# Kernel optimization log

Hardware: AMD Instinct MI355X
Metric: run time of the kernel (lower is better)

The kernel has to match this reference:

```python
import jax, jax.numpy as jnp
import numpy as np

N_NODES = 50000
N_EDGES = 800000
IN_FEATS = 128
H_FEATS = 32
HEADS = 4
OUT_FEATS = 32
OUT_HEADS = 1
NEG_SLOPE = 0.2


def setup_inputs() -> dict:
    key = jax.random.key(0)
    ks = jax.random.split(key, 20)
    s = 0.05
    return {
        "features": jax.random.normal(ks[0], (N_NODES, IN_FEATS), jnp.float32),
        "src": jax.random.randint(ks[1], (N_EDGES,), 0, N_NODES, jnp.int32),
        "dst": jax.random.randint(ks[2], (N_EDGES,), 0, N_NODES, jnp.int32),
        "Ws0": jax.random.normal(ks[3], (IN_FEATS, HEADS * H_FEATS), jnp.float32) * s,
        "bs0": jnp.zeros((HEADS * H_FEATS,), jnp.float32),
        "Wd0": jax.random.normal(ks[4], (IN_FEATS, HEADS * H_FEATS), jnp.float32) * s,
        "bd0": jnp.zeros((HEADS * H_FEATS,), jnp.float32),
        "a0": jax.random.normal(ks[5], (HEADS, H_FEATS), jnp.float32) * s,
        "Ws1": jax.random.normal(ks[6], (HEADS * H_FEATS, HEADS * H_FEATS), jnp.float32) * s,
        "bs1": jnp.zeros((HEADS * H_FEATS,), jnp.float32),
        "Wd1": jax.random.normal(ks[7], (HEADS * H_FEATS, HEADS * H_FEATS), jnp.float32) * s,
        "bd1": jnp.zeros((HEADS * H_FEATS,), jnp.float32),
        "a1": jax.random.normal(ks[8], (HEADS, H_FEATS), jnp.float32) * s,
        "Ws2": jax.random.normal(ks[9], (HEADS * H_FEATS, OUT_HEADS * OUT_FEATS), jnp.float32) * s,
        "bs2": jnp.zeros((OUT_HEADS * OUT_FEATS,), jnp.float32),
        "Wd2": jax.random.normal(ks[10], (HEADS * H_FEATS, OUT_HEADS * OUT_FEATS), jnp.float32) * s,
        "bd2": jnp.zeros((OUT_HEADS * OUT_FEATS,), jnp.float32),
        "a2": jax.random.normal(ks[11], (OUT_HEADS, OUT_FEATS), jnp.float32) * s,
    }


def gatv2_conv(x, src, dst, Ws, bs, Wd, bd, attn, n_nodes):
    """DGL GATv2Conv (share_weights=False, residual=False, no dropout)."""
    heads, f = attn.shape
    feat_src = (x @ Ws + bs).reshape(-1, heads, f)  # [N, H, F]
    feat_dst = (x @ Wd + bd).reshape(-1, heads, f)  # [N, H, F]
    # per-edge GATv2 score: LeakyReLU(Wsrc h_u + Wdst h_v) . a
    e = jax.nn.leaky_relu(feat_src[src] + feat_dst[dst], NEG_SLOPE)  # [E, H, F]
    logits = jnp.einsum("ehf,hf->eh", e, attn)  # [E, H]
    # edge softmax over incoming edges of each dst node
    m = jax.ops.segment_max(logits, dst, num_segments=n_nodes)  # [N, H]
    ex = jnp.exp(logits - m[dst])
    denom = jax.ops.segment_sum(ex, dst, num_segments=n_nodes)  # [N, H]
    alpha = ex / denom[dst]  # [E, H]
    # scatter-aggregate messages
    msg = feat_src[src] * alpha[..., None]  # [E, H, F]
    return jax.ops.segment_sum(msg, dst, num_segments=n_nodes)  # [N, H, F]


def reference(features, src, dst,
              Ws0, bs0, Wd0, bd0, a0,
              Ws1, bs1, Wd1, bd1, a1,
              Ws2, bs2, Wd2, bd2, a2):
    n = features.shape[0]
    h = gatv2_conv(features, src, dst, Ws0, bs0, Wd0, bd0, a0, n)
    h = jax.nn.relu(h.reshape(n, -1))
    h = gatv2_conv(h, src, dst, Ws1, bs1, Wd1, bd1, a1, n)
    h = jax.nn.relu(h.reshape(n, -1))
    h = gatv2_conv(h, src, dst, Ws2, bs2, Wd2, bd2, a2, n)
    return h.mean(axis=1)  # [N, OUT_FEATS]
```

## Files before the change

### kernel.cpp

```cpp
#include <hip/hip_runtime.h>

typedef __attribute__((ext_vector_type(8))) short bf16x8;
typedef __attribute__((ext_vector_type(4))) float f32x4;

#define LOG2E 1.4426950408889634f

#define BINSH 8
#define NBIN 196
#define CHUNK 4096
#define K4CAP 6144

__device__ __forceinline__ unsigned bf_rn(float f) {
    unsigned u = __float_as_uint(f);
    u += 0x7fffu + ((u >> 16) & 1u);
    return u >> 16;
}
__device__ __forceinline__ float bf_lo(unsigned u) { return __uint_as_float(u << 16); }
__device__ __forceinline__ float bf_hi(unsigned u) { return __uint_as_float(u & 0xffff0000u); }

template <int CTRL>
__device__ __forceinline__ float dpp_radd(float x) {
    int t = __builtin_amdgcn_update_dpp(0, __float_as_int(x), CTRL, 0xF, 0xF, true);
    return x + __int_as_float(t);
}
__device__ __forceinline__ float sum8(float p) {
    p = dpp_radd<0x141>(p);
    p = dpp_radd<0x1B>(p);
    p = dpp_radd<0xB1>(p);
    return p;
}
__device__ __forceinline__ float dpp_swap1(float x) {
    return __int_as_float(__builtin_amdgcn_update_dpp(0, __float_as_int(x), 0xB1, 0xF, 0xF, true));
}

__device__ __forceinline__ float fast_exp2(float x) {
#if __has_builtin(__builtin_amdgcn_exp2f)
    return __builtin_amdgcn_exp2f(x);
#else
    return __expf(x * 0.6931471805599453f);
#endif
}


__global__ __launch_bounds__(256) void bin_count(const int* __restrict__ dst,
                                                 int* __restrict__ binCnt, int e) {
    __shared__ int hist[NBIN];
    for (int t = threadIdx.x; t < NBIN; t += 256) hist[t] = 0;
    __syncthreads();
    int base = blockIdx.x * CHUNK;
    int cnt = min(CHUNK, e - base);
    for (int j = threadIdx.x; j < cnt; j += 256)
        atomicAdd(&hist[dst[base + j] >> BINSH], 1);
    __syncthreads();
    for (int t = threadIdx.x; t < NBIN; t += 256)
        if (hist[t]) atomicAdd(&binCnt[t], hist[t]);
}

__global__ void bin_scan(const int* __restrict__ binCnt, int* __restrict__ binBase,
                         int* __restrict__ binCur, int* __restrict__ rowp, int n, int e) {
    int t = threadIdx.x;
    int v = (t < NBIN) ? binCnt[t] : 0;
    int lane = t & 63, w = t >> 6;
    int incl = v;
    for (int off = 1; off < 64; off <<= 1) {
        int tt = __shfl_up(incl, off);
        if (lane >= off) incl += tt;
    }
    __shared__ int wsum[4];
    if (lane == 63) wsum[w] = incl;
    __syncthreads();
    int wpre = 0;
    for (int i = 0; i < w; ++i) wpre += wsum[i];
    int excl = wpre + incl - v;
    if (t < NBIN) { binBase[t] = excl; binCur[t] = excl; }
    if (t == 0) { binBase[NBIN] = e; rowp[n] = e; }
}

__global__ __launch_bounds__(256) void bin_scatter(
    const int* __restrict__ src, const int* __restrict__ dst,
    int* __restrict__ binCur, unsigned* __restrict__ ebin, int e) {
    __shared__ int hist[NBIN];
    __shared__ int seg[NBIN];
    __shared__ int gbase[NBIN];
    __shared__ unsigned pack[CHUNK];
    for (int t = threadIdx.x; t < NBIN; t += 256) hist[t] = 0;
    __syncthreads();
    int base = blockIdx.x * CHUNK;
    int cnt = min(CHUNK, e - base);

    int myb[CHUNK / 256], myr[CHUNK / 256];
    unsigned myw[CHUNK / 256];
    int nmine = 0;
    for (int j = threadIdx.x; j < cnt; j += 256) {
        int d = dst[base + j], s = src[base + j];
        int b = d >> BINSH, dl = d & ((1 << BINSH) - 1);
        int r = atomicAdd(&hist[b], 1);
        myb[nmine] = b; myr[nmine] = r;
        myw[nmine] = ((unsigned)b << 24) | ((unsigned)dl << 16) | (unsigned)s;
        ++nmine;
    }
    __syncthreads();
    if (threadIdx.x == 0) {
        int acc = 0;
        for (int b2 = 0; b2 < NBIN; ++b2) { seg[b2] = acc; acc += hist[b2]; }
    }
    __syncthreads();
    for (int k = 0; k < nmine; ++k)
        pack[seg[myb[k]] + myr[k]] = myw[k];
    __syncthreads();
    if (threadIdx.x < NBIN && hist[threadIdx.x])
        gbase[threadIdx.x] = atomicAdd(&binCur[threadIdx.x], hist[threadIdx.x]);
    __syncthreads();
    for (int j = threadIdx.x; j < cnt; j += 256) {
        unsigned wv = pack[j];
        int b = wv >> 24;
        ebin[gbase[b] + (j - seg[b])] = wv;
    }
}

__global__ __launch_bounds__(256) void csr_build(
    const unsigned* __restrict__ ebin, const int* __restrict__ binBase,
    int* __restrict__ rowp, int* __restrict__ csrc, int n) {
    __shared__ int hist[256];
    __shared__ int seg[256];
    __shared__ unsigned stage[K4CAP];
    int b = blockIdx.x;
    int e0 = binBase[b], e1 = binBase[b + 1];
    int n0 = b << BINSH;
    int nn = min(256, n - n0);
    for (int t = threadIdx.x; t < 256; t += 256) hist[t] = 0;
    __syncthreads();
    for (int i = e0 + threadIdx.x; i < e1; i += 256) {
        unsigned wv = ebin[i];
        atomicAdd(&hist[(wv >> 16) & 255], 1);
        int off = i - e0;
        if (off < K4CAP) stage[off] = wv;
    }
    __syncthreads();
    if (threadIdx.x < 64) {
        int l = threadIdx.x;
        int s = 0, loc[4];
#pragma unroll
        for (int k = 0; k < 4; ++k) { loc[k] = s; s += hist[l * 4 + k]; }
        int incl = s;
        for (int off = 1; off < 64; off <<= 1) {
            int tt = __shfl_up(incl, off);
            if (l >= off) incl += tt;
        }
        int excl = incl - s;
#pragma unroll
        for (int k = 0; k < 4; ++k) seg[l * 4 + k] = excl + loc[k];
    }
    __syncthreads();
    for (int t = threadIdx.x; t < nn; t += 256) rowp[n0 + t] = e0 + seg[t];
    for (int t = threadIdx.x; t < 256; t += 256) hist[t] = seg[t];
    __syncthreads();
    for (int i = e0 + threadIdx.x; i < e1; i += 256) {
        int off = i - e0;
        unsigned wv = (off < K4CAP) ? stage[off] : ebin[i];
        int dl = (wv >> 16) & 255;
        int pos = e0 + atomicAdd(&hist[dl], 1);
        csrc[pos] = (int)(wv & 0xFFFFu);
    }
}


__global__ void convert_feat(const float* __restrict__ x, unsigned short* __restrict__ o, int n4) {
    int i = blockIdx.x * blockDim.x + threadIdx.x;
    if (i < n4) {
        float4 v = *(const float4*)(x + (size_t)i * 4);
        ushort4 r;
        r.x = (unsigned short)bf_rn(v.x); r.y = (unsigned short)bf_rn(v.y);
        r.z = (unsigned short)bf_rn(v.z); r.w = (unsigned short)bf_rn(v.w);
        *(ushort4*)(o + (size_t)i * 4) = r;
    }
}

__global__ void transpose_all(
    const float* __restrict__ Ws0, const float* __restrict__ Wd0,
    const float* __restrict__ Ws1, const float* __restrict__ Wd1,
    const float* __restrict__ Ws2, const float* __restrict__ Wd2,
    unsigned short* __restrict__ wt0, unsigned short* __restrict__ wt1,
    unsigned short* __restrict__ wt2) {
    int gid = blockIdx.x * blockDim.x + threadIdx.x;
    if (gid < 65536) {
        int l = gid >> 15, loc = gid & 32767;
        int c = loc >> 7, k = loc & 127;
        const float* W = (c < 128) ? (l ? Ws1 : Ws0) : (l ? Wd1 : Wd0);
        int cc = c & 127;
        float v = W[(size_t)k * 128 + cc];
        (l ? wt1 : wt0)[loc] = (unsigned short)bf_rn(v);
    } else if (gid < 65536 + 8192) {
        int loc = gid - 65536;
        int c = loc >> 7, k = loc & 127;
        const float* W = (c < 32) ? Ws2 : Wd2;
        int cc = (c < 32) ? c : c - 32;
        float v = W[(size_t)k * 32 + cc];
        wt2[loc] = (unsigned short)bf_rn(v);
    }
}


template <int COLS2>
__global__ __launch_bounds__(256) void gemm_dual2(
    const unsigned short* __restrict__ xb, const unsigned short* __restrict__ wt,
    const float* __restrict__ bs, const float* __restrict__ bd,
    unsigned short* __restrict__ fs, unsigned short* __restrict__ fd,
    int n, int nch) {
    constexpr int C  = COLS2 / 2;
    constexpr int NC = COLS2 / 64;

    const int lane = threadIdx.x & 63;
    const int m = lane & 15, quad = lane >> 4;
    const int gwid = blockIdx.x * 4 + (threadIdx.x >> 6);
    const int nwaves = gridDim.x * 4;
    const int cs = gwid % NC;
    const int cstride = nwaves / NC;

    float biasv[4];
#pragma unroll
    for (int ct = 0; ct < 4; ++ct) {
        int col = cs * 64 + ct * 16 + m;
        biasv[ct] = (col < C) ? bs[col] : bd[col - C];
    }

    for (int chunk = gwid / NC; chunk < nch; chunk += cstride) {
        const size_t r0 = (size_t)chunk * 64;

        f32x4 acc[4][4];
#pragma unroll
        for (int rt = 0; rt < 4; ++rt)
#pragma unroll
            for (int ct = 0; ct < 4; ++ct) acc[rt][ct] = (f32x4){0.f, 0.f, 0.f, 0.f};

#pragma unroll
        for (int ks = 0; ks < 4; ++ks) {
            const int ko = ks * 32 + quad * 8;
            bf16x8 a[4], b[4];
#pragma unroll
            for (int rt = 0; rt < 4; ++rt)
                a[rt] = *(const bf16x8*)(xb + (r0 + rt * 16 + m) * 128 + ko);
#pragma unroll
            for (int ct = 0; ct < 4; ++ct)
                b[ct] = *(const bf16x8*)(wt + (size_t)(cs * 64 + ct * 16 + m) * 128 + ko);
#pragma unroll
            for (int rt = 0; rt < 4; ++rt)
#pragma unroll
                for (int ct = 0; ct < 4; ++ct)
                    acc[rt][ct] = __builtin_amdgcn_mfma_f32_16x16x32_bf16(a[rt], b[ct], acc[rt][ct], 0, 0, 0);
        }

        const int odd = m & 1;
#pragma unroll
        for (int ct = 0; ct < 4; ++ct) {
            int colE = cs * 64 + ct * 16 + (m & ~1);
            unsigned short* ptr = (colE < C) ? fs : fd;
            int cc = (colE < C) ? colE : colE - C;
#pragma unroll
            for (int rt = 0; rt < 4; ++rt) {
                float v0 = acc[rt][ct][0] + biasv[ct];
                float v1 = acc[rt][ct][1] + biasv[ct];
                float v2 = acc[rt][ct][2] + biasv[ct];
                float v3 = acc[rt][ct][3] + biasv[ct];
                float s0 = dpp_swap1(v0), s1 = dpp_swap1(v1);
                float s2 = dpp_swap1(v2), s3 = dpp_swap1(v3);
                float aLo = odd ? s2 : v0, aHi = odd ? v2 : s0;
                float bLo = odd ? s3 : v1, bHi = odd ? v3 : s1;
                int rowA = (int)r0 + rt * 16 + quad * 4 + (odd ? 2 : 0);
                unsigned pa = (bf_rn(aHi) << 16) | bf_rn(aLo);
                unsigned pb = (bf_rn(bHi) << 16) | bf_rn(bLo);
                if (rowA < n)     *(unsigned*)(ptr + (size_t)rowA * C + cc)       = pa;
                if (rowA + 1 < n) *(unsigned*)(ptr + ((size_t)rowA + 1) * C + cc) = pb;
            }
        }
    }
}


#define EDGE_BODY(u, mval)                                          \
    do {                                                            \
        float x0 = bf_lo((u).x), x1 = bf_hi((u).x);                 \
        float x2 = bf_lo((u).y), x3 = bf_hi((u).y);                 \
        float t0 = x0 + fd0, t1 = x1 + fd1;                         \
        float t2 = x2 + fd2, t3 = x3 + fd3;                         \
        float p = a060 * t0;                                        \
        p = fmaf(a040, fabsf(t0), p);                               \
        p = fmaf(a061, t1, p); p = fmaf(a041, fabsf(t1), p);        \
        p = fmaf(a062, t2, p); p = fmaf(a042, fabsf(t2), p);        \
        p = fmaf(a063, t3, p); p = fmaf(a043, fabsf(t3), p);        \
        p = sum8(p);                                                \
        float ex = fast_exp2(p) * (mval);                           \
        denom += ex;                                                \
        acc0 = fmaf(ex, x0, acc0); acc1 = fmaf(ex, x1, acc1);       \
        acc2 = fmaf(ex, x2, acc2); acc3 = fmaf(ex, x3, acc3);       \
    } while (0)

__global__ __launch_bounds__(256) void conv128(
    const unsigned short* __restrict__ fs, const unsigned short* __restrict__ fd,
    const float* __restrict__ attn, const int* __restrict__ rowp,
    const int* __restrict__ csrc, unsigned short* __restrict__ out, int n) {
    const int nwaves = gridDim.x * 4;
    const int wid0 = blockIdx.x * 4 + (threadIdx.x >> 6);
    const int lane = threadIdx.x & 63;
    const int half = lane >> 5;
    const int q = lane & 31;

    float4 av = *(const float4*)(attn + q * 4);
    const float a060 = av.x * 0.6f * LOG2E, a040 = av.x * 0.4f * LOG2E;
    const float a061 = av.y * 0.6f * LOG2E, a041 = av.y * 0.4f * LOG2E;
    const float a062 = av.z * 0.6f * LOG2E, a042 = av.z * 0.4f * LOG2E;
    const float a063 = av.w * 0.6f * LOG2E, a043 = av.w * 0.4f * LOG2E;

    for (int wid = wid0; wid < n; wid += nwaves) {
        uint2 ud = *(const uint2*)(fd + (size_t)wid * 128 + q * 4);
        float fd0 = bf_lo(ud.x), fd1 = bf_hi(ud.x);
        float fd2 = bf_lo(ud.y), fd3 = bf_hi(ud.y);
        int rs = rowp[wid], re = rowp[wid + 1];
        float acc0 = 0.f, acc1 = 0.f, acc2 = 0.f, acc3 = 0.f, denom = 0.f;

        int i = rs;
        for (; i + 3 < re; i += 4) {
            int sA = csrc[i + half];
            int sB = csrc[i + 2 + half];
            uint2 uA = *(const uint2*)(fs + ((size_t)sA << 7) + q * 4);
            uint2 uB = *(const uint2*)(fs + ((size_t)sB << 7) + q * 4);
            EDGE_BODY(uA, 1.0f);
            EDGE_BODY(uB, 1.0f);
        }
        for (; i + 1 < re; i += 2) {
            int s = csrc[i + half];
            uint2 u = *(const uint2*)(fs + ((size_t)s << 7) + q * 4);
            EDGE_BODY(u, 1.0f);
        }
        if (i < re) {
            int s = csrc[i];
            uint2 u = *(const uint2*)(fs + ((size_t)s << 7) + q * 4);
            float mval = half ? 0.f : 1.f;
            EDGE_BODY(u, mval);
        }
        acc0 += __shfl_xor(acc0, 32); acc1 += __shfl_xor(acc1, 32);
        acc2 += __shfl_xor(acc2, 32); acc3 += __shfl_xor(acc3, 32);
        denom += __shfl_xor(denom, 32);
        float inv = (re > rs) ? 1.f / denom : 0.f;
        float r0 = fmaxf(acc0 * inv, 0.f), r1 = fmaxf(acc1 * inv, 0.f);
        float r2 = fmaxf(acc2 * inv, 0.f), r3 = fmaxf(acc3 * inv, 0.f);
        if (half == 0) {
            uint2 o;
            o.x = (bf_rn(r1) << 16) | bf_rn(r0);
            o.y = (bf_rn(r3) << 16) | bf_rn(r2);
            ((uint2*)(out + (size_t)wid * 128))[q] = o;
        }
    }
}

__global__ __launch_bounds__(256) void conv32(
    const unsigned short* __restrict__ fs, const unsigned short* __restrict__ fd,
    const float* __restrict__ attn, const int* __restrict__ rowp,
    const int* __restrict__ csrc, float* __restrict__ out, int n) {
    const int nwaves = gridDim.x * 4;
    const int wid0 = blockIdx.x * 4 + (threadIdx.x >> 6);
    const int lane = threadIdx.x & 63;
    const int g = lane >> 3;
    const int c = lane & 7;

    float4 av = *(const float4*)(attn + c * 4);
    const float a060 = av.x * 0.6f * LOG2E, a040 = av.x * 0.4f * LOG2E;
    const float a061 = av.y * 0.6f * LOG2E, a041 = av.y * 0.4f * LOG2E;
    const float a062 = av.z * 0.6f * LOG2E, a042 = av.z * 0.4f * LOG2E;
    const float a063 = av.w * 0.6f * LOG2E, a043 = av.w * 0.4f * LOG2E;

    for (int wid = wid0; wid < n; wid += nwaves) {
        uint2 ud = *(const uint2*)(fd + (size_t)wid * 32 + c * 4);
        float fd0 = bf_lo(ud.x), fd1 = bf_hi(ud.x);
        float fd2 = bf_lo(ud.y), fd3 = bf_hi(ud.y);
        int rs = rowp[wid], re = rowp[wid + 1];
        float acc0 = 0.f, acc1 = 0.f, acc2 = 0.f, acc3 = 0.f, denom = 0.f;

        int i = rs;
        for (; i + 7 < re; i += 8) {
            int s = csrc[i + g];
            uint2 u = *(const uint2*)(fs + ((size_t)s << 5) + c * 4);
            EDGE_BODY(u, 1.0f);
        }
        if (i < re) {
            int idx = i + g;
            int s = csrc[min(idx, re - 1)];
            uint2 u = *(const uint2*)(fs + ((size_t)s << 5) + c * 4);
            float mval = (idx < re) ? 1.f : 0.f;
            EDGE_BODY(u, mval);
        }
        acc0 = dpp_radd<0x128>(acc0); acc1 = dpp_radd<0x128>(acc1);
        acc2 = dpp_radd<0x128>(acc2); acc3 = dpp_radd<0x128>(acc3);
        denom = dpp_radd<0x128>(denom);
        acc0 += __shfl_xor(acc0, 16); acc1 += __shfl_xor(acc1, 16);
        acc2 += __shfl_xor(acc2, 16); acc3 += __shfl_xor(acc3, 16);
        denom += __shfl_xor(denom, 16);
        acc0 += __shfl_xor(acc0, 32); acc1 += __shfl_xor(acc1, 32);
        acc2 += __shfl_xor(acc2, 32); acc3 += __shfl_xor(acc3, 32);
        denom += __shfl_xor(denom, 32);
        float inv = (re > rs) ? 1.f / denom : 0.f;
        if (lane < 8) {
            float4 o;
            o.x = acc0 * inv; o.y = acc1 * inv;
            o.z = acc2 * inv; o.w = acc3 * inv;
            *(float4*)(out + (size_t)wid * 32 + c * 4) = o;
        }
    }
}


extern "C" void kernel_launch(void* const* d_in, const int* in_sizes, int n_in,
                              void* d_out, int out_size, void* d_ws, size_t ws_size,
                              hipStream_t stream) {
    const float* feats = (const float*)d_in[0];
    const int*   src   = (const int*)d_in[1];
    const int*   dst   = (const int*)d_in[2];
    const float* Ws0 = (const float*)d_in[3],  *bs0 = (const float*)d_in[4];
    const float* Wd0 = (const float*)d_in[5],  *bd0 = (const float*)d_in[6];
    const float* a0  = (const float*)d_in[7];
    const float* Ws1 = (const float*)d_in[8],  *bs1 = (const float*)d_in[9];
    const float* Wd1 = (const float*)d_in[10], *bd1 = (const float*)d_in[11];
    const float* a1  = (const float*)d_in[12];
    const float* Ws2 = (const float*)d_in[13], *bs2 = (const float*)d_in[14];
    const float* Wd2 = (const float*)d_in[15], *bd2 = (const float*)d_in[16];
    const float* a2  = (const float*)d_in[17];

    const int N = in_sizes[0] / 128;
    const int E = in_sizes[1];
    const int nch = (N + 63) / 64;
    const int NPAD = nch * 64;

    char* ws = (char*)d_ws;
    const size_t featB = (size_t)NPAD * 128 * 2;
    unsigned short* xb  = (unsigned short*)(ws);
    unsigned short* hb  = (unsigned short*)(ws + featB);
    unsigned short* fsb = (unsigned short*)(ws + 2 * featB);
    unsigned short* fdb = (unsigned short*)(ws + 3 * featB);
    char* p = ws + 4 * featB;
    unsigned short* wt0 = (unsigned short*)p; p += 256 * 128 * 2;
    unsigned short* wt1 = (unsigned short*)p; p += 256 * 128 * 2;
    unsigned short* wt2 = (unsigned short*)p; p += 64 * 128 * 2;
    int* rowp    = (int*)p;      p += ((size_t)(N + 1) * 4 + 255) / 256 * 256;
    int* binCnt  = (int*)p;      p += (NBIN * 4 + 255) / 256 * 256;
    int* binBase = (int*)p;      p += ((NBIN + 1) * 4 + 255) / 256 * 256;
    int* binCur  = (int*)p;      p += (NBIN * 4 + 255) / 256 * 256;
    unsigned* ebin = (unsigned*)p; p += (size_t)E * 4;
    int* csrc    = (int*)p;

    const int nchunks = (E + CHUNK - 1) / CHUNK;

    hipMemsetAsync(binCnt, 0, NBIN * 4, stream);
    bin_count<<<nchunks, 256, 0, stream>>>(dst, binCnt, E);
    bin_scan<<<1, 256, 0, stream>>>(binCnt, binBase, binCur, rowp, N, E);
    bin_scatter<<<nchunks, 256, 0, stream>>>(src, dst, binCur, ebin, E);
    csr_build<<<NBIN, 256, 0, stream>>>(ebin, binBase, rowp, csrc, N);

    const int n4 = N * 128 / 4;
    convert_feat<<<(n4 + 255) / 256, 256, 0, stream>>>(feats, xb, n4);
    transpose_all<<<(73728 + 255) / 256, 256, 0, stream>>>(Ws0, Wd0, Ws1, Wd1, Ws2, Wd2, wt0, wt1, wt2);

    const int g256 = nch;
    const int g64  = (nch + 3) / 4;
    const int convGrid = 2048;

    gemm_dual2<256><<<g256, 256, 0, stream>>>(xb, wt0, bs0, bd0, fsb, fdb, N, nch);
    conv128<<<convGrid, 256, 0, stream>>>(fsb, fdb, a0, rowp, csrc, hb, N);
    gemm_dual2<256><<<g256, 256, 0, stream>>>(hb, wt1, bs1, bd1, fsb, fdb, N, nch);
    conv128<<<convGrid, 256, 0, stream>>>(fsb, fdb, a1, rowp, csrc, hb, N);
    gemm_dual2<64><<<g64, 256, 0, stream>>>(hb, wt2, bs2, bd2, fsb, fdb, N, nch);
    conv32<<<convGrid, 256, 0, stream>>>(fsb, fdb, a2, rowp, csrc, (float*)d_out, N);
}
```

Measured before the change: 295.9 us.

## Fuse preprocessing launches and overlap edge binning with first-layer GEMM

Merges the memset, feature conversion and weight transpose into one prep kernel. The dst-bin histogram and the first GEMM now run in a single heterogeneous launch, with some blocks counting and the others computing. The separate bin_scan kernel is dropped: both bin_scatter and csr_build recompute the bin prefix sum locally from binCnt. This cuts the launch count and serial dependencies in the preprocessing phase, at the cost of redundant scans and a scatter that reads dst twice.

```diff
diff --git a/kernel.cpp b/kernel.cpp
--- a/kernel.cpp
+++ b/kernel.cpp
@@ -42,178 +42,54 @@
 }
 
 
-__global__ __launch_bounds__(256) void bin_count(const int* __restrict__ dst,
-                                                 int* __restrict__ binCnt, int e) {
-    __shared__ int hist[NBIN];
-    for (int t = threadIdx.x; t < NBIN; t += 256) hist[t] = 0;
-    __syncthreads();
-    int base = blockIdx.x * CHUNK;
-    int cnt = min(CHUNK, e - base);
-    for (int j = threadIdx.x; j < cnt; j += 256)
-        atomicAdd(&hist[dst[base + j] >> BINSH], 1);
-    __syncthreads();
-    for (int t = threadIdx.x; t < NBIN; t += 256)
-        if (hist[t]) atomicAdd(&binCnt[t], hist[t]);
-}
-
-__global__ void bin_scan(const int* __restrict__ binCnt, int* __restrict__ binBase,
-                         int* __restrict__ binCur, int* __restrict__ rowp, int n, int e) {
-    int t = threadIdx.x;
-    int v = (t < NBIN) ? binCnt[t] : 0;
-    int lane = t & 63, w = t >> 6;
-    int incl = v;
-    for (int off = 1; off < 64; off <<= 1) {
-        int tt = __shfl_up(incl, off);
-        if (lane >= off) incl += tt;
-    }
-    __shared__ int wsum[4];
-    if (lane == 63) wsum[w] = incl;
-    __syncthreads();
-    int wpre = 0;
-    for (int i = 0; i < w; ++i) wpre += wsum[i];
-    int excl = wpre + incl - v;
-    if (t < NBIN) { binBase[t] = excl; binCur[t] = excl; }
-    if (t == 0) { binBase[NBIN] = e; rowp[n] = e; }
-}
-
-__global__ __launch_bounds__(256) void bin_scatter(
-    const int* __restrict__ src, const int* __restrict__ dst,
-    int* __restrict__ binCur, unsigned* __restrict__ ebin, int e) {
-    __shared__ int hist[NBIN];
-    __shared__ int seg[NBIN];
-    __shared__ int gbase[NBIN];
-    __shared__ unsigned pack[CHUNK];
-    for (int t = threadIdx.x; t < NBIN; t += 256) hist[t] = 0;
-    __syncthreads();
-    int base = blockIdx.x * CHUNK;
-    int cnt = min(CHUNK, e - base);
-
-    int myb[CHUNK / 256], myr[CHUNK / 256];
-    unsigned myw[CHUNK / 256];
-    int nmine = 0;
-    for (int j = threadIdx.x; j < cnt; j += 256) {
-        int d = dst[base + j], s = src[base + j];
-        int b = d >> BINSH, dl = d & ((1 << BINSH) - 1);
-        int r = atomicAdd(&hist[b], 1);
-        myb[nmine] = b; myr[nmine] = r;
-        myw[nmine] = ((unsigned)b << 24) | ((unsigned)dl << 16) | (unsigned)s;
-        ++nmine;
-    }
-    __syncthreads();
-    if (threadIdx.x == 0) {
-        int acc = 0;
-        for (int b2 = 0; b2 < NBIN; ++b2) { seg[b2] = acc; acc += hist[b2]; }
-    }
-    __syncthreads();
-    for (int k = 0; k < nmine; ++k)
-        pack[seg[myb[k]] + myr[k]] = myw[k];
-    __syncthreads();
-    if (threadIdx.x < NBIN && hist[threadIdx.x])
-        gbase[threadIdx.x] = atomicAdd(&binCur[threadIdx.x], hist[threadIdx.x]);
-    __syncthreads();
-    for (int j = threadIdx.x; j < cnt; j += 256) {
-        unsigned wv = pack[j];
-        int b = wv >> 24;
-        ebin[gbase[b] + (j - seg[b])] = wv;
-    }
-}
-
-__global__ __launch_bounds__(256) void csr_build(
-    const unsigned* __restrict__ ebin, const int* __restrict__ binBase,
-    int* __restrict__ rowp, int* __restrict__ csrc, int n) {
-    __shared__ int hist[256];
-    __shared__ int seg[256];
-    __shared__ unsigned stage[K4CAP];
-    int b = blockIdx.x;
-    int e0 = binBase[b], e1 = binBase[b + 1];
-    int n0 = b << BINSH;
-    int nn = min(256, n - n0);
-    for (int t = threadIdx.x; t < 256; t += 256) hist[t] = 0;
-    __syncthreads();
-    for (int i = e0 + threadIdx.x; i < e1; i += 256) {
-        unsigned wv = ebin[i];
-        atomicAdd(&hist[(wv >> 16) & 255], 1);
-        int off = i - e0;
-        if (off < K4CAP) stage[off] = wv;
-    }
-    __syncthreads();
-    if (threadIdx.x < 64) {
-        int l = threadIdx.x;
-        int s = 0, loc[4];
-#pragma unroll
-        for (int k = 0; k < 4; ++k) { loc[k] = s; s += hist[l * 4 + k]; }
-        int incl = s;
-        for (int off = 1; off < 64; off <<= 1) {
-            int tt = __shfl_up(incl, off);
-            if (l >= off) incl += tt;
-        }
-        int excl = incl - s;
-#pragma unroll
-        for (int k = 0; k < 4; ++k) seg[l * 4 + k] = excl + loc[k];
-    }
-    __syncthreads();
-    for (int t = threadIdx.x; t < nn; t += 256) rowp[n0 + t] = e0 + seg[t];
-    for (int t = threadIdx.x; t < 256; t += 256) hist[t] = seg[t];
-    __syncthreads();
-    for (int i = e0 + threadIdx.x; i < e1; i += 256) {
-        int off = i - e0;
-        unsigned wv = (off < K4CAP) ? stage[off] : ebin[i];
-        int dl = (wv >> 16) & 255;
-        int pos = e0 + atomicAdd(&hist[dl], 1);
-        csrc[pos] = (int)(wv & 0xFFFFu);
-    }
-}
-
-
-__global__ void convert_feat(const float* __restrict__ x, unsigned short* __restrict__ o, int n4) {
-    int i = blockIdx.x * blockDim.x + threadIdx.x;
-    if (i < n4) {
-        float4 v = *(const float4*)(x + (size_t)i * 4);
-        ushort4 r;
-        r.x = (unsigned short)bf_rn(v.x); r.y = (unsigned short)bf_rn(v.y);
-        r.z = (unsigned short)bf_rn(v.z); r.w = (unsigned short)bf_rn(v.w);
-        *(ushort4*)(o + (size_t)i * 4) = r;
-    }
-}
-
-__global__ void transpose_all(
+__global__ __launch_bounds__(256) void prep(
+    const float* __restrict__ x, unsigned short* __restrict__ xb, int n4,
     const float* __restrict__ Ws0, const float* __restrict__ Wd0,
     const float* __restrict__ Ws1, const float* __restrict__ Wd1,
     const float* __restrict__ Ws2, const float* __restrict__ Wd2,
     unsigned short* __restrict__ wt0, unsigned short* __restrict__ wt1,
-    unsigned short* __restrict__ wt2) {
+    unsigned short* __restrict__ wt2, int* __restrict__ binCnt,
+    int* __restrict__ binOff) {
     int gid = blockIdx.x * blockDim.x + threadIdx.x;
-    if (gid < 65536) {
-        int l = gid >> 15, loc = gid & 32767;
-        int c = loc >> 7, k = loc & 127;
-        const float* W = (c < 128) ? (l ? Ws1 : Ws0) : (l ? Wd1 : Wd0);
-        int cc = c & 127;
-        float v = W[(size_t)k * 128 + cc];
-        (l ? wt1 : wt0)[loc] = (unsigned short)bf_rn(v);
-    } else if (gid < 65536 + 8192) {
-        int loc = gid - 65536;
-        int c = loc >> 7, k = loc & 127;
-        const float* W = (c < 32) ? Ws2 : Wd2;
-        int cc = (c < 32) ? c : c - 32;
-        float v = W[(size_t)k * 32 + cc];
-        wt2[loc] = (unsigned short)bf_rn(v);
+    if (gid < NBIN) { binCnt[gid] = 0; binOff[gid] = 0; }
+    if (gid < n4) {
+        float4 v = *(const float4*)(x + (size_t)gid * 4);
+        ushort4 r;
+        r.x = (unsigned short)bf_rn(v.x); r.y = (unsigned short)bf_rn(v.y);
+        r.z = (unsigned short)bf_rn(v.z); r.w = (unsigned short)bf_rn(v.w);
+        *(ushort4*)(xb + (size_t)gid * 4) = r;
+    } else {
+        int g = gid - n4;
+        if (g < 65536) {
+            int l = g >> 15, loc = g & 32767;
+            int c = loc >> 7, k = loc & 127;
+            const float* W = (c < 128) ? (l ? Ws1 : Ws0) : (l ? Wd1 : Wd0);
+            int cc = c & 127;
+            float v = W[(size_t)k * 128 + cc];
+            (l ? wt1 : wt0)[loc] = (unsigned short)bf_rn(v);
+        } else if (g < 65536 + 8192) {
+            int loc = g - 65536;
+            int c = loc >> 7, k = loc & 127;
+            const float* W = (c < 32) ? Ws2 : Wd2;
+            int cc = (c < 32) ? c : c - 32;
+            float v = W[(size_t)k * 32 + cc];
+            wt2[loc] = (unsigned short)bf_rn(v);
+        }
     }
 }
 
 
 template <int COLS2>
-__global__ __launch_bounds__(256) void gemm_dual2(
+__device__ __forceinline__ void gemm_core(
     const unsigned short* __restrict__ xb, const unsigned short* __restrict__ wt,
     const float* __restrict__ bs, const float* __restrict__ bd,
     unsigned short* __restrict__ fs, unsigned short* __restrict__ fd,
-    int n, int nch) {
+    int n, int nch, int gwid, int nwaves) {
     constexpr int C  = COLS2 / 2;
     constexpr int NC = COLS2 / 64;
 
     const int lane = threadIdx.x & 63;
     const int m = lane & 15, quad = lane >> 4;
-    const int gwid = blockIdx.x * 4 + (threadIdx.x >> 6);
-    const int nwaves = gridDim.x * 4;
     const int cs = gwid % NC;
     const int cstride = nwaves / NC;
 
@@ -273,6 +149,179 @@
                 if (rowA + 1 < n) *(unsigned*)(ptr + ((size_t)rowA + 1) * C + cc) = pb;
             }
         }
+    }
+}
+
+template <int COLS2>
+__global__ __launch_bounds__(256) void gemm_dual2(
+    const unsigned short* __restrict__ xb, const unsigned short* __restrict__ wt,
+    const float* __restrict__ bs, const float* __restrict__ bd,
+    unsigned short* __restrict__ fs, unsigned short* __restrict__ fd,
+    int n, int nch) {
+    gemm_core<COLS2>(xb, wt, bs, bd, fs, fd, n, nch,
+                     blockIdx.x * 4 + (threadIdx.x >> 6), gridDim.x * 4);
+}
+
+
+__global__ __launch_bounds__(256) void count_gemm0(
+    const int* __restrict__ dst, int* __restrict__ binCnt, int e, int nchunks,
+    const unsigned short* __restrict__ xb, const unsigned short* __restrict__ wt,
+    const float* __restrict__ bs, const float* __restrict__ bd,
+    unsigned short* __restrict__ fs, unsigned short* __restrict__ fd,
+    int n, int nch) {
+    if ((int)blockIdx.x < nchunks) {
+        __shared__ int hist[NBIN];
+        for (int t = threadIdx.x; t < NBIN; t += 256) hist[t] = 0;
+        __syncthreads();
+        int base = blockIdx.x * CHUNK;
+        int cnt = min(CHUNK, e - base);
+        for (int j = threadIdx.x; j < cnt; j += 256)
+            atomicAdd(&hist[dst[base + j] >> BINSH], 1);
+        __syncthreads();
+        for (int t = threadIdx.x; t < NBIN; t += 256)
+            if (hist[t]) atomicAdd(&binCnt[t], hist[t]);
+    } else {
+        int bid = blockIdx.x - nchunks;
+        gemm_core<256>(xb, wt, bs, bd, fs, fd, n, nch,
+                       bid * 4 + (threadIdx.x >> 6), (gridDim.x - nchunks) * 4);
+    }
+}
+
+
+__global__ __launch_bounds__(256) void bin_scatter(
+    const int* __restrict__ src, const int* __restrict__ dst,
+    const int* __restrict__ binCnt, int* __restrict__ binOff,
+    unsigned* __restrict__ ebin, int e) {
+    __shared__ int hist[256];
+    __shared__ int seg[256];
+    __shared__ int bbase[256];
+    __shared__ int gbase[NBIN];
+    __shared__ unsigned pack[CHUNK];
+    for (int t = threadIdx.x; t < 256; t += 256) hist[t] = 0;
+    if (threadIdx.x < 64) {
+        int l = threadIdx.x;
+        int s = 0, loc[4];
+#pragma unroll
+        for (int k = 0; k < 4; ++k) {
+            int idx = l * 4 + k;
+            int v = (idx < NBIN) ? binCnt[idx] : 0;
+            loc[k] = s; s += v;
+        }
+        int incl = s;
+        for (int off = 1; off < 64; off <<= 1) {
+            int tt = __shfl_up(incl, off);
+            if (l >= off) incl += tt;
+        }
+        int excl = incl - s;
+#pragma unroll
+        for (int k = 0; k < 4; ++k) bbase[l * 4 + k] = excl + loc[k];
+    }
+    __syncthreads();
+    int base = blockIdx.x * CHUNK;
+    int cnt = min(CHUNK, e - base);
+
+    for (int j = threadIdx.x; j < cnt; j += 256)
+        atomicAdd(&hist[dst[base + j] >> BINSH], 1);
+    __syncthreads();
+    if (threadIdx.x < 64) {
+        int l = threadIdx.x;
+        int s = 0, loc[4];
+#pragma unroll
+        for (int k = 0; k < 4; ++k) { loc[k] = s; s += hist[l * 4 + k]; }
+        int incl = s;
+        for (int off = 1; off < 64; off <<= 1) {
+            int tt = __shfl_up(incl, off);
+            if (l >= off) incl += tt;
+        }
+        int excl = incl - s;
+#pragma unroll
+        for (int k = 0; k < 4; ++k) seg[l * 4 + k] = excl + loc[k];
+    }
+    __syncthreads();
+    if (threadIdx.x < NBIN && hist[threadIdx.x])
+        gbase[threadIdx.x] = bbase[threadIdx.x] + atomicAdd(&binOff[threadIdx.x], hist[threadIdx.x]);
+    __syncthreads();
+    for (int t = threadIdx.x; t < 256; t += 256) hist[t] = seg[t];
+    __syncthreads();
+    for (int j = threadIdx.x; j < cnt; j += 256) {
+        int d = dst[base + j], s = src[base + j];
+        int b = d >> BINSH, dl = d & ((1 << BINSH) - 1);
+        int pos = atomicAdd(&hist[b], 1);
+        pack[pos] = ((unsigned)b << 24) | ((unsigned)dl << 16) | (unsigned)s;
+    }
+    __syncthreads();
+    for (int j = threadIdx.x; j < cnt; j += 256) {
+        unsigned wv = pack[j];
+        int b = wv >> 24;
+        ebin[gbase[b] + (j - seg[b])] = wv;
+    }
+}
+
+
+__global__ __launch_bounds__(256) void csr_build(
+    const unsigned* __restrict__ ebin, const int* __restrict__ binCnt,
+    int* __restrict__ rowp, int* __restrict__ csrc, int n) {
+    __shared__ int hist[256];
+    __shared__ int seg[256];
+    __shared__ int bbase[257];
+    __shared__ unsigned stage[K4CAP];
+    int b = blockIdx.x;
+    if (threadIdx.x < 64) {
+        int l = threadIdx.x;
+        int s = 0, loc[4];
+#pragma unroll
+        for (int k = 0; k < 4; ++k) {
+            int idx = l * 4 + k;
+            int v = (idx < NBIN) ? binCnt[idx] : 0;
+            loc[k] = s; s += v;
+        }
+        int incl = s;
+        for (int off = 1; off < 64; off <<= 1) {
+            int tt = __shfl_up(incl, off);
+            if (l >= off) incl += tt;
+        }
+        int excl = incl - s;
+#pragma unroll
+        for (int k = 0; k < 4; ++k) bbase[l * 4 + k] = excl + loc[k];
+        if (l == 63) bbase[256] = incl;
+    }
+    for (int t = threadIdx.x; t < 256; t += 256) hist[t] = 0;
+    __syncthreads();
+    int e0 = bbase[b], e1 = bbase[b + 1];
+    int n0 = b << BINSH;
+    int nn = min(256, n - n0);
+    if (b == NBIN - 1 && threadIdx.x == 0) rowp[n] = bbase[NBIN];
+    for (int i = e0 + threadIdx.x; i < e1; i += 256) {
+        unsigned wv = ebin[i];
+        atomicAdd(&hist[(wv >> 16) & 255], 1);
+        int off = i - e0;
+        if (off < K4CAP) stage[off] = wv;
+    }
+    __syncthreads();
+    if (threadIdx.x < 64) {
+        int l = threadIdx.x;
+        int s = 0, loc[4];
+#pragma unroll
+        for (int k = 0; k < 4; ++k) { loc[k] = s; s += hist[l * 4 + k]; }
+        int incl = s;
+        for (int off = 1; off < 64; off <<= 1) {
+            int tt = __shfl_up(incl, off);
+            if (l >= off) incl += tt;
+        }
+        int excl = incl - s;
+#pragma unroll
+        for (int k = 0; k < 4; ++k) seg[l * 4 + k] = excl + loc[k];
+    }
+    __syncthreads();
+    for (int t = threadIdx.x; t < nn; t += 256) rowp[n0 + t] = e0 + seg[t];
+    for (int t = threadIdx.x; t < 256; t += 256) hist[t] = seg[t];
+    __syncthreads();
+    for (int i = e0 + threadIdx.x; i < e1; i += 256) {
+        int off = i - e0;
+        unsigned wv = (off < K4CAP) ? stage[off] : ebin[i];
+        int dl = (wv >> 16) & 255;
+        int pos = e0 + atomicAdd(&hist[dl], 1);
+        csrc[pos] = (int)(wv & 0xFFFFu);
     }
 }
 
@@ -442,28 +491,26 @@
     unsigned short* wt2 = (unsigned short*)p; p += 64 * 128 * 2;
     int* rowp    = (int*)p;      p += ((size_t)(N + 1) * 4 + 255) / 256 * 256;
     int* binCnt  = (int*)p;      p += (NBIN * 4 + 255) / 256 * 256;
-    int* binBase = (int*)p;      p += ((NBIN + 1) * 4 + 255) / 256 * 256;
-    int* binCur  = (int*)p;      p += (NBIN * 4 + 255) / 256 * 256;
+    int* binOff  = (int*)p;      p += (NBIN * 4 + 255) / 256 * 256;
     unsigned* ebin = (unsigned*)p; p += (size_t)E * 4;
     int* csrc    = (int*)p;
 
     const int nchunks = (E + CHUNK - 1) / CHUNK;
-
-    hipMemsetAsync(binCnt, 0, NBIN * 4, stream);
-    bin_count<<<nchunks, 256, 0, stream>>>(dst, binCnt, E);
-    bin_scan<<<1, 256, 0, stream>>>(binCnt, binBase, binCur, rowp, N, E);
-    bin_scatter<<<nchunks, 256, 0, stream>>>(src, dst, binCur, ebin, E);
-    csr_build<<<NBIN, 256, 0, stream>>>(ebin, binBase, rowp, csrc, N);
-
     const int n4 = N * 128 / 4;
-    convert_feat<<<(n4 + 255) / 256, 256, 0, stream>>>(feats, xb, n4);
-    transpose_all<<<(73728 + 255) / 256, 256, 0, stream>>>(Ws0, Wd0, Ws1, Wd1, Ws2, Wd2, wt0, wt1, wt2);
 
     const int g256 = nch;
     const int g64  = (nch + 3) / 4;
     const int convGrid = 2048;
 
-    gemm_dual2<256><<<g256, 256, 0, stream>>>(xb, wt0, bs0, bd0, fsb, fdb, N, nch);
+    prep<<<(n4 + 73728 + 255) / 256, 256, 0, stream>>>(
+        feats, xb, n4, Ws0, Wd0, Ws1, Wd1, Ws2, Wd2, wt0, wt1, wt2, binCnt, binOff);
+
+    count_gemm0<<<nchunks + g256, 256, 0, stream>>>(
+        dst, binCnt, E, nchunks, xb, wt0, bs0, bd0, fsb, fdb, N, nch);
+
+    bin_scatter<<<nchunks, 256, 0, stream>>>(src, dst, binCnt, binOff, ebin, E);
+    csr_build<<<NBIN, 256, 0, stream>>>(ebin, binCnt, rowp, csrc, N);
+
     conv128<<<convGrid, 256, 0, stream>>>(fsb, fdb, a0, rowp, csrc, hb, N);
     gemm_dual2<256><<<g256, 256, 0, stream>>>(hb, wt1, bs1, bd1, fsb, fdb, N, nch);
     conv128<<<convGrid, 256, 0, stream>>>(fsb, fdb, a1, rowp, csrc, hb, N);
```

Measured after the change: 282.4 us, median of 2. -4.6%, faster.
